# Optimization experiments

Hardware: AMD Instinct MI355X
Metric: run time of the kernel (lower is better)

Reference implementation:

```python
import jax, jax.numpy as jnp
import numpy as np

NLAT, NLON = 64, 64
CIN = 512
HEADS = 8


def _cc_weights(n):
    # Clenshaw-Curtis quadrature weights on [-1, 1] for nodes cos(k*pi/(n-1)),
    # as used by torch-harmonics for the 'equiangular' grid. Weights sum to 2.
    N = n - 1
    theta = np.pi * np.arange(n) / N
    m = N // 2
    j = np.arange(1, m + 1)
    b = np.where(2 * j == N, 1.0, 2.0)
    S = (b / (4.0 * j ** 2 - 1.0))[None, :] * np.cos(2.0 * j[None, :] * theta[:, None])
    w = 1.0 - S.sum(axis=1)
    c = np.full(n, 2.0)
    c[0] = 1.0
    c[-1] = 1.0
    return c * w / N


def _log_quad_weights(nlat, nlon):
    # _precompute_latitudes flips nodes/weights; then 2*pi*w/nlon tiled over lon.
    w = _cc_weights(nlat)[::-1].copy()
    qw = 2.0 * np.pi * w / nlon                       # (nlat,)
    qw = np.tile(qw[:, None], (1, nlon)).reshape(-1)  # (nlat*nlon,)
    return jnp.asarray(np.log(qw), dtype=jnp.float32)


def setup_inputs() -> dict:
    key = jax.random.key(0)
    ks = jax.random.split(key, 5)
    s_qkv = float(np.sqrt(3.0 / CIN))   # scale for q/k/v 1x1-conv weights
    s_proj = float(np.sqrt(3.0 / CIN))  # out_channels == CIN
    u = lambda k, sh, s: jax.random.uniform(k, sh, jnp.float32, -s, s)
    return dict(
        query=jax.random.normal(ks[0], (1, CIN, NLAT, NLON), jnp.float32),
        q_w=u(ks[1], (CIN, CIN), s_qkv), q_b=jnp.zeros((CIN,), jnp.float32),
        k_w=u(ks[2], (CIN, CIN), s_qkv), k_b=jnp.zeros((CIN,), jnp.float32),
        v_w=u(ks[3], (CIN, CIN), s_qkv), v_b=jnp.zeros((CIN,), jnp.float32),
        p_w=u(ks[4], (CIN, CIN), s_proj), p_b=jnp.zeros((CIN,), jnp.float32),
        log_quad_weights=_log_quad_weights(NLAT, NLON),
    )


def reference(query, q_w, q_b, k_w, k_b, v_w, v_b, p_w, p_b, log_quad_weights):
    B, C, H, W = query.shape
    hd = C // HEADS  # head dim (k_channels == out_channels == in_channels)

    def proj_tokens(x, w, b):
        # 1x1 conv == channel matmul, then split heads and flatten H*W tokens
        y = jnp.einsum('bihw,oi->bohw', x, w) + b[None, :, None, None]
        return y.reshape(B, HEADS, -1, H, W).transpose(0, 1, 3, 4, 2).reshape(B, HEADS, H * W, -1)

    q = proj_tokens(query, q_w, q_b)  # (B, heads, HW, hd)
    k = proj_tokens(query, k_w, k_b)  # self-attention: key/value default to query
    v = proj_tokens(query, v_w, v_b)

    scale = 1.0 / jnp.sqrt(jnp.asarray(hd, dtype=q.dtype))
    # additive log-quadrature bias over keys (broadcast over batch/head/query)
    logits = jnp.einsum('bhqd,bhkd->bhqk', q, k) * scale + log_quad_weights[None, None, None, :]
    attn = jax.nn.softmax(logits, axis=-1)
    out = jnp.einsum('bhqk,bhkd->bhqd', attn, v)          # (B, heads, HW, hd)
    out = out.transpose(0, 1, 3, 2).reshape(B, HEADS * hd, H, W)
    return jnp.einsum('bihw,oi->bohw', out, p_w) + p_b[None, :, None, None]
```

## Files before the change

### kernel.cpp

```cpp
#include <hip/hip_runtime.h>

typedef unsigned short u16;
typedef unsigned int u32;
typedef __bf16 bf16x8 __attribute__((ext_vector_type(8)));
typedef float f32x4 __attribute__((ext_vector_type(4)));
typedef unsigned short u16x4 __attribute__((ext_vector_type(4)));

#define LOG2E 1.4426950408889634f

#if __has_builtin(__builtin_amdgcn_exp2f)
#define EXP2F(x) __builtin_amdgcn_exp2f(x)
#else
#define EXP2F(x) exp2f(x)
#endif

__device__ __forceinline__ u16 f2bf(float f) {
    union { float f; u32 u; } a; a.f = f;
    u32 u = a.u;
    u += 0x7FFFu + ((u >> 16) & 1u);
    return (u16)(u >> 16);
}
__device__ __forceinline__ bf16x8 ldg8(const u16* p) {
    return *reinterpret_cast<const bf16x8*>(p);
}
#if __has_builtin(__builtin_amdgcn_cvt_pk_bf16_f32)
__device__ __forceinline__ u32 pack2(float a, float b) {
    auto r = __builtin_amdgcn_cvt_pk_bf16_f32(a, b);
    return __builtin_bit_cast(u32, r);
}
#else
__device__ __forceinline__ u32 pack2(float a, float b) {
    u32 ua = __float_as_uint(a) + 0x8000u;
    u32 ub = __float_as_uint(b) + 0x8000u;
    return __builtin_amdgcn_perm(ub, ua, 0x07060302);
}
#endif
__device__ __forceinline__ void async16(const void* g, void* l) {
    __builtin_amdgcn_global_load_lds(
        (const __attribute__((address_space(1))) u32*)g,
        (__attribute__((address_space(3))) u32*)l, 16, 0, 0);
}

#define MFMA16(a, b, c) __builtin_amdgcn_mfma_f32_16x16x32_bf16((a), (b), (c), 0, 0, 0)

__global__ __launch_bounds__(256) void prep(const float* __restrict__ X,
                                            u16* __restrict__ Xt,
                                            const float* __restrict__ s0,
                                            const float* __restrict__ s1,
                                            const float* __restrict__ s2,
                                            const float* __restrict__ s3,
                                            u16* __restrict__ Wqkv,
                                            u16* __restrict__ Wp,
                                            const float* __restrict__ lqw,
                                            float* __restrict__ lqw2g) {
    __shared__ u16 tile[64][65];
    const int tid = threadIdx.x;
    const int y = blockIdx.y;

    if (y < 8) {
        const int t0 = blockIdx.x * 64;
        const int c0 = y * 64;
#pragma unroll
        for (int i = 0; i < 16; ++i) {
            int idx = tid + i * 256;
            int r = idx >> 6, cc = idx & 63;
            tile[r][cc] = f2bf(X[(size_t)(c0 + r) * 4096 + t0 + cc]);
        }
        __syncthreads();
#pragma unroll
        for (int i = 0; i < 16; ++i) {
            int idx = tid + i * 256;
            int tr = idx >> 6, cc = idx & 63;
            Xt[(size_t)(t0 + tr) * 512 + c0 + cc] = tile[cc][tr];
        }
    } else if (y < 12) {
        const int m = y - 8;
        const float* s = (m == 0) ? s0 : (m == 1) ? s1 : (m == 2) ? s2 : s3;
        u16* d = (m == 3) ? Wp : Wqkv + (size_t)m * 262144;
#pragma unroll
        for (int j = 0; j < 4; ++j) {
            int i = blockIdx.x * 1024 + j * 256 + tid;
            float4 v = reinterpret_cast<const float4*>(s)[i];
            u16x4 o;
            o[0] = f2bf(v.x); o[1] = f2bf(v.y); o[2] = f2bf(v.z); o[3] = f2bf(v.w);
            reinterpret_cast<u16x4*>(d)[i] = o;
        }
    } else {
        if (blockIdx.x < 4) {
            int i = blockIdx.x * 256 + tid;
            float4 v = reinterpret_cast<const float4*>(lqw)[i];
            v.x *= LOG2E; v.y *= LOG2E; v.z *= LOG2E; v.w *= LOG2E;
            reinterpret_cast<float4*>(lqw2g)[i] = v;
        }
    }
}

__global__ __launch_bounds__(512, 2) void qkv_gemm(const u16* __restrict__ Wqkv,
                                                   const u16* __restrict__ Xt,
                                                   const float* __restrict__ qb,
                                                   const float* __restrict__ kb,
                                                   const float* __restrict__ vb,
                                                   u16* __restrict__ Qt,
                                                   u16* __restrict__ Kt,
                                                   u16* __restrict__ Vp) {
    __shared__ __align__(16) u16 Al[2][128 * 32];
    __shared__ __align__(16) u16 Bl[2][128 * 32];

    const int tid = threadIdx.x;
    const int w = tid >> 6, lane = tid & 63;
    const int quad = lane >> 4, lm = lane & 15;
    const int wm = w & 1, wn = w >> 1;
    const int n0 = blockIdx.x * 128;
    const int my = blockIdx.y;
    const int m0 = my * 128;

    const int arow = lane >> 2;
    const int sch = (lane & 3) ^ ((lane >> 3) & 3);
    const u16* agp = Wqkv + (size_t)(m0 + w * 16 + arow) * 512 + sch * 8;
    const u16* bgp = Xt + (size_t)(n0 + w * 16 + arow) * 512 + sch * 8;

    async16(agp, &Al[0][w * 16 * 32]);
    async16(bgp, &Bl[0][w * 16 * 32]);
    agp += 32; bgp += 32;

    const int FOFF = lm * 64 + ((quad ^ ((lm >> 1) & 3)) << 4);

    f32x4 acc[4][2];
#pragma unroll
    for (int mt = 0; mt < 4; ++mt)
#pragma unroll
        for (int bt = 0; bt < 2; ++bt) acc[mt][bt] = (f32x4){0.f, 0.f, 0.f, 0.f};

    __syncthreads();

    for (int s = 0; s < 16; ++s) {
        const int buf = s & 1;
        if (s < 15) {
            async16(agp, &Al[buf ^ 1][w * 16 * 32]);
            async16(bgp, &Bl[buf ^ 1][w * 16 * 32]);
            agp += 32; bgp += 32;
        }
        const char* Ab = (const char*)&Al[buf][0];
        const char* Bb = (const char*)&Bl[buf][0];
        bf16x8 af[4], bfr[2];
#pragma unroll
        for (int mt = 0; mt < 4; ++mt)
            af[mt] = *(const bf16x8*)(Ab + wm * 4096 + mt * 1024 + FOFF);
#pragma unroll
        for (int bt = 0; bt < 2; ++bt)
            bfr[bt] = *(const bf16x8*)(Bb + wn * 2048 + bt * 1024 + FOFF);
#pragma unroll
        for (int mt = 0; mt < 4; ++mt)
#pragma unroll
            for (int bt = 0; bt < 2; ++bt)
                acc[mt][bt] = MFMA16(af[mt], bfr[bt], acc[mt][bt]);
        __syncthreads();
    }

    const int mat = my >> 2;
    const float* bias = (mat == 0) ? qb : (mat == 1) ? kb : vb;
    const int chbase = (my & 3) * 128 + wm * 64 + quad * 4;

    if (mat < 2) {
        u16* out = mat ? Kt : Qt;
        const float sc = mat ? 1.0f : 0.125f * LOG2E;
#pragma unroll
        for (int mt = 0; mt < 4; ++mt) {
            const int ch = chbase + mt * 16;
            float4 bv = *(const float4*)(bias + ch);
            float bvf[4] = {bv.x, bv.y, bv.z, bv.w};
#pragma unroll
            for (int bt = 0; bt < 2; ++bt) {
                int tok = n0 + wn * 32 + bt * 16 + lm;
                u16x4 pk;
#pragma unroll
                for (int r = 0; r < 4; ++r)
                    pk[r] = f2bf((acc[mt][bt][r] + bvf[r]) * sc);
                *(u16x4*)(out + (size_t)tok * 512 + ch) = pk;
            }
        }
    } else {
#pragma unroll
        for (int mt = 0; mt < 4; ++mt) {
            const int ch = chbase + mt * 16;
            float4 bv = *(const float4*)(bias + ch);
            float bvf[4] = {bv.x, bv.y, bv.z, bv.w};
#pragma unroll
            for (int bt = 0; bt < 2; ++bt) {
                int g = bt * 16 + lm;
                int col = n0 + wn * 32 + 8 * ((g >> 2) & 3) + 4 * ((g >> 4) & 1) + (g & 3);
#pragma unroll
                for (int r = 0; r < 4; ++r)
                    Vp[(size_t)(ch + r) * 4096 + col] = f2bf(acc[mt][bt][r] + bvf[r]);
            }
        }
    }
}

__global__ __launch_bounds__(256, 2) void out_gemm(const u16* __restrict__ Wp,
                                                   const u16* __restrict__ Ot,
                                                   const float* __restrict__ pb,
                                                   float* __restrict__ out) {
    __shared__ __align__(16) u16 Al[2][128 * 32];
    __shared__ __align__(16) u16 Bl[2][64 * 32];

    const int tid = threadIdx.x;
    const int w = tid >> 6, lane = tid & 63;
    const int quad = lane >> 4, lm = lane & 15;
    const int wm = w & 1, wn = w >> 1;
    const int n0 = blockIdx.x * 64;
    const int m0 = blockIdx.y * 128;

    const int arow = lane >> 2;
    const int sch = (lane & 3) ^ ((lane >> 3) & 3);
    const u16* agp0 = Wp + (size_t)(m0 + w * 16 + arow) * 512 + sch * 8;
    const u16* agp1 = agp0 + (size_t)64 * 512;
    const u16* bgp = Ot + (size_t)(n0 + w * 16 + arow) * 512 + sch * 8;

    async16(agp0, &Al[0][w * 16 * 32]);
    async16(agp1, &Al[0][(64 + w * 16) * 32]);
    async16(bgp, &Bl[0][w * 16 * 32]);
    agp0 += 32; agp1 += 32; bgp += 32;

    const int FOFF = lm * 64 + ((quad ^ ((lm >> 1) & 3)) << 4);

    f32x4 acc[4][2];
#pragma unroll
    for (int mt = 0; mt < 4; ++mt)
#pragma unroll
        for (int bt = 0; bt < 2; ++bt) acc[mt][bt] = (f32x4){0.f, 0.f, 0.f, 0.f};

    __syncthreads();

    for (int s = 0; s < 16; ++s) {
        const int buf = s & 1;
        if (s < 15) {
            async16(agp0, &Al[buf ^ 1][w * 16 * 32]);
            async16(agp1, &Al[buf ^ 1][(64 + w * 16) * 32]);
            async16(bgp, &Bl[buf ^ 1][w * 16 * 32]);
            agp0 += 32; agp1 += 32; bgp += 32;
        }
        const char* Ab = (const char*)&Al[buf][0];
        const char* Bb = (const char*)&Bl[buf][0];
        bf16x8 af[4], bfr[2];
#pragma unroll
        for (int mt = 0; mt < 4; ++mt)
            af[mt] = *(const bf16x8*)(Ab + wm * 4096 + mt * 1024 + FOFF);
#pragma unroll
        for (int bt = 0; bt < 2; ++bt)
            bfr[bt] = *(const bf16x8*)(Bb + wn * 2048 + bt * 1024 + FOFF);
#pragma unroll
        for (int mt = 0; mt < 4; ++mt)
#pragma unroll
            for (int bt = 0; bt < 2; ++bt)
                acc[mt][bt] = MFMA16(af[mt], bfr[bt], acc[mt][bt]);
        __syncthreads();
    }

#pragma unroll
    for (int mt = 0; mt < 4; ++mt) {
        const int ch = m0 + wm * 64 + mt * 16 + quad * 4;
        float4 bv = *(const float4*)(pb + ch);
        float bvf[4] = {bv.x, bv.y, bv.z, bv.w};
#pragma unroll
        for (int bt = 0; bt < 2; ++bt) {
            int tok = n0 + wn * 32 + bt * 16 + lm;
#pragma unroll
            for (int r = 0; r < 4; ++r)
                out[(size_t)(ch + r) * 4096 + tok] = acc[mt][bt][r] + bvf[r];
        }
    }
}

#define WAITVM(N) asm volatile("s_waitcnt vmcnt(" #N ")" ::: "memory")

__global__ __launch_bounds__(256, 2) void flash_attn(const u16* __restrict__ Qt,
                                                     const u16* __restrict__ Kt,
                                                     const u16* __restrict__ Vp,
                                                     const float* __restrict__ lqw2g,
                                                     u16* __restrict__ Ot) {
    __shared__ __align__(16) char smem[65536];

    const int tid = threadIdx.x;
    const int w = tid >> 6, lane = tid & 63;
    const int quad = lane >> 4, lm = lane & 15;
    const int bid = blockIdx.x;
    const int h = bid & 7, hq = h * 64;
    const int q0 = (bid >> 3) * 64;
    const int kstart = w * 1024;

    char* kvw = smem + w * 16384;

    const int srow = lane >> 3;
    const int schunk = (lane & 7) ^ srow;
    const u16* kg = Kt + (size_t)(kstart + srow) * 512 + hq + schunk * 8;
    const u16* vg = Vp + (size_t)(hq + 2 * srow + (schunk >> 2)) * 4096 +
                    kstart + (schunk & 3) * 8;

    bf16x8 bq0[4], bq1[4];
#pragma unroll
    for (int s = 0; s < 4; ++s) {
        const u16* qb = Qt + (size_t)(q0 + s * 16 + lm) * 512 + hq + quad * 8;
        bq0[s] = ldg8(qb);
        bq1[s] = ldg8(qb + 32);
    }

    f32x4 breg0 = *(const f32x4*)(lqw2g + kstart + quad * 4);
    f32x4 breg1 = *(const f32x4*)(lqw2g + kstart + 16 + quad * 4);
    const float* bptr = lqw2g + kstart + 32 + quad * 4;

    const int A0 = lm * 128 + ((quad ^ (lm & 7)) << 4);
    const int A1 = A0 ^ 64;
    const int AV = (lm >> 1) * 128 +
                   (((4 * (lm & 1) + quad) ^ ((lm >> 1) & 7)) << 4);

#define STAGEBLK(DST)                                                          \
    {                                                                          \
        char* nb = (DST);                                                      \
        async16(kg, nb);                                                       \
        async16(kg + 8 * 512, nb + 1024);                                      \
        async16(kg + 16 * 512, nb + 2048);                                     \
        async16(kg + 24 * 512, nb + 3072);                                     \
        async16(vg, nb + 4096);                                                \
        async16(vg + (size_t)16 * 4096, nb + 5120);                            \
        async16(vg + (size_t)32 * 4096, nb + 6144);                            \
        async16(vg + (size_t)48 * 4096, nb + 7168);                            \
        kg += 32 * 512; vg += 32;                                              \
    }

    STAGEBLK(kvw)
    STAGEBLK(kvw + 8192)

    union { u32 u[4]; bf16x8 v; } onesu;
    onesu.u[0] = onesu.u[1] = onesu.u[2] = onesu.u[3] = 0x3F803F80u;
    const bf16x8 onesv = onesu.v;

    f32x4 acc_o[4][4];
#pragma unroll
    for (int mt = 0; mt < 4; ++mt)
#pragma unroll
        for (int s = 0; s < 4; ++s) acc_o[mt][s] = (f32x4){0.f, 0.f, 0.f, 0.f};
    f32x4 acc_l[4];
#pragma unroll
    for (int s = 0; s < 4; ++s) acc_l[s] = (f32x4){0.f, 0.f, 0.f, 0.f};

    int bufsel = 0;

#define BODY(WN, DOBIAS, DOSTAGE)                                              \
    {                                                                          \
        WAITVM(WN);                                                            \
        const char* Kb = kvw + bufsel;                                         \
        const char* Vb = Kb + 4096;                                            \
        bf16x8 k00 = *(const bf16x8*)(Kb + A0);                                \
        bf16x8 k01 = *(const bf16x8*)(Kb + A1);                                \
        bf16x8 k10 = *(const bf16x8*)(Kb + 2048 + A0);                         \
        bf16x8 k11 = *(const bf16x8*)(Kb + 2048 + A1);                         \
        bf16x8 vf0 = *(const bf16x8*)(Vb + AV);                                \
        bf16x8 vf1 = *(const bf16x8*)(Vb + 1024 + AV);                         \
        bf16x8 vf2 = *(const bf16x8*)(Vb + 2048 + AV);                         \
        bf16x8 vf3 = *(const bf16x8*)(Vb + 3072 + AV);                         \
        u32 bbu[4][4];                                                         \
        _Pragma("unroll")                                                      \
        for (int s = 0; s < 4; ++s) {                                          \
            f32x4 a = MFMA16(k00, bq0[s], breg0);                              \
            a = MFMA16(k01, bq1[s], a);                                        \
            bbu[s][0] = pack2(EXP2F(a[0]), EXP2F(a[1]));                       \
            bbu[s][1] = pack2(EXP2F(a[2]), EXP2F(a[3]));                       \
        }                                                                      \
        _Pragma("unroll")                                                      \
        for (int s = 0; s < 4; ++s) {                                          \
            f32x4 a = MFMA16(k10, bq0[s], breg1);                              \
            a = MFMA16(k11, bq1[s], a);                                        \
            bbu[s][2] = pack2(EXP2F(a[0]), EXP2F(a[1]));                       \
            bbu[s][3] = pack2(EXP2F(a[2]), EXP2F(a[3]));                       \
        }                                                                      \
        if (DOBIAS) {                                                          \
            breg0 = *(const f32x4*)(bptr);                                     \
            breg1 = *(const f32x4*)(bptr + 16);                                \
            bptr += 32;                                                        \
        }                                                                      \
        union { u32 u[4]; bf16x8 v; } bb[4];                                   \
        _Pragma("unroll")                                                      \
        for (int s = 0; s < 4; ++s) {                                          \
            bb[s].u[0] = bbu[s][0]; bb[s].u[1] = bbu[s][1];                    \
            bb[s].u[2] = bbu[s][2]; bb[s].u[3] = bbu[s][3];                    \
        }                                                                      \
        _Pragma("unroll")                                                      \
        for (int s = 0; s < 4; ++s) {                                          \
            acc_o[0][s] = MFMA16(vf0, bb[s].v, acc_o[0][s]);                   \
            acc_o[1][s] = MFMA16(vf1, bb[s].v, acc_o[1][s]);                   \
            acc_o[2][s] = MFMA16(vf2, bb[s].v, acc_o[2][s]);                   \
            acc_o[3][s] = MFMA16(vf3, bb[s].v, acc_o[3][s]);                   \
            acc_l[s] = MFMA16(onesv, bb[s].v, acc_l[s]);                       \
        }                                                                      \
        if (DOSTAGE) STAGEBLK(kvw + bufsel)                                    \
        bufsel ^= 8192;                                                        \
    }

    BODY(8, true, true)
    for (int t = 1; t < 30; ++t)
        BODY(10, true, true)
    BODY(10, true, false)
    BODY(2, false, false)

#undef BODY
#undef STAGEBLK

    __syncthreads();
    float* mbuf = (float*)smem;
    if (w != 0) {
        float* ob = mbuf + (w - 1) * 4096;
#pragma unroll
        for (int s = 0; s < 4; ++s) {
            const int r = s * 16 + lm;
#pragma unroll
            for (int mt = 0; mt < 4; ++mt) {
                const int sl = (mt * 4 + quad) ^ lm;
                *(f32x4*)(ob + r * 64 + sl * 4) = acc_o[mt][s];
            }
        }
        if (quad == 0) {
#pragma unroll
            for (int s = 0; s < 4; ++s)
                mbuf[12288 + (w - 1) * 64 + s * 16 + lm] = acc_l[s][0];
        }
    }
    __syncthreads();
    if (w != 0) return;

#pragma unroll
    for (int s = 0; s < 4; ++s) {
        const int r = s * 16 + lm;
        float lsum = acc_l[s][0];
#pragma unroll
        for (int p = 0; p < 3; ++p)
            lsum += mbuf[12288 + p * 64 + r];
        const float inv = 1.0f / lsum;
#pragma unroll
        for (int mt = 0; mt < 4; ++mt) {
            const int sl = (mt * 4 + quad) ^ lm;
            f32x4 o = acc_o[mt][s];
#pragma unroll
            for (int p = 0; p < 3; ++p)
                o += *(const f32x4*)(mbuf + p * 4096 + r * 64 + sl * 4);
            u16x4 pkv;
#pragma unroll
            for (int r2 = 0; r2 < 4; ++r2)
                pkv[r2] = f2bf(o[r2] * inv);
            *reinterpret_cast<u16x4*>(Ot + (size_t)(q0 + r) * 512 +
                                      hq + mt * 16 + quad * 4) = pkv;
        }
    }
}

extern "C" void kernel_launch(void* const* d_in, const int* in_sizes, int n_in,
                              void* d_out, int out_size, void* d_ws, size_t ws_size,
                              hipStream_t stream) {
    (void)in_sizes; (void)n_in; (void)out_size; (void)ws_size;
    const float* X   = (const float*)d_in[0];
    const float* qw  = (const float*)d_in[1];
    const float* qb  = (const float*)d_in[2];
    const float* kw  = (const float*)d_in[3];
    const float* kb  = (const float*)d_in[4];
    const float* vw  = (const float*)d_in[5];
    const float* vb  = (const float*)d_in[6];
    const float* pw  = (const float*)d_in[7];
    const float* pb  = (const float*)d_in[8];
    const float* lqw = (const float*)d_in[9];

    const size_t E = (size_t)4096 * 512;
    const size_t WE = (size_t)512 * 512;
    u16* Xt    = (u16*)d_ws;
    u16* Qt    = Xt + E;
    u16* Kt    = Qt + E;
    u16* Vp    = Kt + E;
    u16* Wqkv  = Vp + E;
    u16* Wp    = Wqkv + 3 * WE;
    float* lqw2g = (float*)(Wp + WE);
    u16* Ot    = Xt;

    prep<<<dim3(64, 13), dim3(256), 0, stream>>>(X, Xt, qw, kw, vw, pw,
                                                 Wqkv, Wp, lqw, lqw2g);
    qkv_gemm<<<dim3(32, 12), dim3(512), 0, stream>>>(Wqkv, Xt, qb, kb, vb, Qt, Kt, Vp);
    flash_attn<<<dim3(512), dim3(256), 0, stream>>>(Qt, Kt, Vp, lqw2g, Ot);
    out_gemm<<<dim3(64, 4), dim3(256), 0, stream>>>(Wp, Ot, pb, (float*)d_out);
}
```

Measured before the change: 78.59 us.

## Split flash attention keys across 8 waves and load V directly from global

The attention block grows from 4 to 8 waves, each handling 512 keys instead of 1024, and the launch bounds rise to 512 threads with 4 blocks per CU. V fragments are now read straight from global memory into registers rather than staged through LDS, so only K is double-buffered in shared memory. The K prefetch is issued earlier in each iteration. The cross-wave reduction runs in two passes to fit the smaller shared buffer. This is meant to raise parallelism and occupancy and cut LDS traffic, at the cost of uncached-looking global V loads on the critical path, register pressure under the tighter launch bound, and extra synchronisation in the reduction.

```diff
diff --git a/kernel.cpp b/kernel.cpp
--- a/kernel.cpp
+++ b/kernel.cpp
@@ -274,7 +274,7 @@
 
 #define WAITVM(N) asm volatile("s_waitcnt vmcnt(" #N ")" ::: "memory")
 
-__global__ __launch_bounds__(256, 2) void flash_attn(const u16* __restrict__ Qt,
+__global__ __launch_bounds__(512, 4) void flash_attn(const u16* __restrict__ Qt,
                                                      const u16* __restrict__ Kt,
                                                      const u16* __restrict__ Vp,
                                                      const float* __restrict__ lqw2g,
@@ -287,15 +287,15 @@
     const int bid = blockIdx.x;
     const int h = bid & 7, hq = h * 64;
     const int q0 = (bid >> 3) * 64;
-    const int kstart = w * 1024;
-
-    char* kvw = smem + w * 16384;
+    const int kstart = w * 512;
+
+    char* kvw = smem + w * 8192;
 
     const int srow = lane >> 3;
     const int schunk = (lane & 7) ^ srow;
     const u16* kg = Kt + (size_t)(kstart + srow) * 512 + hq + schunk * 8;
-    const u16* vg = Vp + (size_t)(hq + 2 * srow + (schunk >> 2)) * 4096 +
-                    kstart + (schunk & 3) * 8;
+
+    const u16* vp = Vp + (size_t)(hq + lm) * 4096 + kstart + quad * 8;
 
     bf16x8 bq0[4], bq1[4];
 #pragma unroll
@@ -311,25 +311,19 @@
 
     const int A0 = lm * 128 + ((quad ^ (lm & 7)) << 4);
     const int A1 = A0 ^ 64;
-    const int AV = (lm >> 1) * 128 +
-                   (((4 * (lm & 1) + quad) ^ ((lm >> 1) & 7)) << 4);
-
-#define STAGEBLK(DST)                                                          \
+
+#define STAGEK(DST)                                                            \
     {                                                                          \
         char* nb = (DST);                                                      \
         async16(kg, nb);                                                       \
         async16(kg + 8 * 512, nb + 1024);                                      \
         async16(kg + 16 * 512, nb + 2048);                                     \
         async16(kg + 24 * 512, nb + 3072);                                     \
-        async16(vg, nb + 4096);                                                \
-        async16(vg + (size_t)16 * 4096, nb + 5120);                            \
-        async16(vg + (size_t)32 * 4096, nb + 6144);                            \
-        async16(vg + (size_t)48 * 4096, nb + 7168);                            \
-        kg += 32 * 512; vg += 32;                                              \
-    }
-
-    STAGEBLK(kvw)
-    STAGEBLK(kvw + 8192)
+        kg += 32 * 512;                                                        \
+    }
+
+    STAGEK(kvw)
+    STAGEK(kvw + 4096)
 
     union { u32 u[4]; bf16x8 v; } onesu;
     onesu.u[0] = onesu.u[1] = onesu.u[2] = onesu.u[3] = 0x3F803F80u;
@@ -350,15 +344,15 @@
     {                                                                          \
         WAITVM(WN);                                                            \
         const char* Kb = kvw + bufsel;                                         \
-        const char* Vb = Kb + 4096;                                            \
+        bf16x8 vf0 = ldg8(vp);                                                 \
+        bf16x8 vf1 = ldg8(vp + (size_t)16 * 4096);                             \
+        bf16x8 vf2 = ldg8(vp + (size_t)32 * 4096);                             \
+        bf16x8 vf3 = ldg8(vp + (size_t)48 * 4096);                             \
+        vp += 32;                                                              \
         bf16x8 k00 = *(const bf16x8*)(Kb + A0);                                \
         bf16x8 k01 = *(const bf16x8*)(Kb + A1);                                \
         bf16x8 k10 = *(const bf16x8*)(Kb + 2048 + A0);                         \
         bf16x8 k11 = *(const bf16x8*)(Kb + 2048 + A1);                         \
-        bf16x8 vf0 = *(const bf16x8*)(Vb + AV);                                \
-        bf16x8 vf1 = *(const bf16x8*)(Vb + 1024 + AV);                         \
-        bf16x8 vf2 = *(const bf16x8*)(Vb + 2048 + AV);                         \
-        bf16x8 vf3 = *(const bf16x8*)(Vb + 3072 + AV);                         \
         u32 bbu[4][4];                                                         \
         _Pragma("unroll")                                                      \
         for (int s = 0; s < 4; ++s) {                                          \
@@ -379,6 +373,7 @@
             breg1 = *(const f32x4*)(bptr + 16);                                \
             bptr += 32;                                                        \
         }                                                                      \
+        if (DOSTAGE) STAGEK(kvw + bufsel)                                      \
         union { u32 u[4]; bf16x8 v; } bb[4];                                   \
         _Pragma("unroll")                                                      \
         for (int s = 0; s < 4; ++s) {                                          \
@@ -393,36 +388,64 @@
             acc_o[3][s] = MFMA16(vf3, bb[s].v, acc_o[3][s]);                   \
             acc_l[s] = MFMA16(onesv, bb[s].v, acc_l[s]);                       \
         }                                                                      \
-        if (DOSTAGE) STAGEBLK(kvw + bufsel)                                    \
-        bufsel ^= 8192;                                                        \
-    }
-
-    BODY(8, true, true)
-    for (int t = 1; t < 30; ++t)
-        BODY(10, true, true)
-    BODY(10, true, false)
-    BODY(2, false, false)
+        bufsel ^= 4096;                                                        \
+    }
+
+    BODY(4, true, true)
+    for (int t = 1; t < 15; ++t)
+        BODY(10, true, (t <= 13))
+    BODY(6, false, false)
 
 #undef BODY
-#undef STAGEBLK
+#undef STAGEK
 
     __syncthreads();
     float* mbuf = (float*)smem;
+    float* lbuf = mbuf + 7 * 2048;
+
     if (w != 0) {
-        float* ob = mbuf + (w - 1) * 4096;
+        float* ob = mbuf + (w - 1) * 2048;
 #pragma unroll
         for (int s = 0; s < 4; ++s) {
             const int r = s * 16 + lm;
 #pragma unroll
-            for (int mt = 0; mt < 4; ++mt) {
-                const int sl = (mt * 4 + quad) ^ lm;
-                *(f32x4*)(ob + r * 64 + sl * 4) = acc_o[mt][s];
+            for (int mt = 0; mt < 2; ++mt) {
+                const int sl = (mt * 4 + quad) ^ (lm & 7);
+                *(f32x4*)(ob + r * 32 + sl * 4) = acc_o[mt][s];
             }
         }
-        if (quad == 0) {
+        if (quad == 0)
 #pragma unroll
             for (int s = 0; s < 4; ++s)
-                mbuf[12288 + (w - 1) * 64 + s * 16 + lm] = acc_l[s][0];
+                lbuf[(w - 1) * 64 + s * 16 + lm] = acc_l[s][0];
+    }
+    __syncthreads();
+    if (w == 0) {
+#pragma unroll
+        for (int s = 0; s < 4; ++s) {
+            const int r = s * 16 + lm;
+#pragma unroll
+            for (int p = 0; p < 7; ++p) {
+#pragma unroll
+                for (int mt = 0; mt < 2; ++mt) {
+                    const int sl = (mt * 4 + quad) ^ (lm & 7);
+                    acc_o[mt][s] += *(const f32x4*)(mbuf + p * 2048 + r * 32 + sl * 4);
+                }
+                acc_l[s][0] += lbuf[p * 64 + r];
+            }
+        }
+    }
+    __syncthreads();
+    if (w != 0) {
+        float* ob = mbuf + (w - 1) * 2048;
+#pragma unroll
+        for (int s = 0; s < 4; ++s) {
+            const int r = s * 16 + lm;
+#pragma unroll
+            for (int mt = 2; mt < 4; ++mt) {
+                const int sl = ((mt - 2) * 4 + quad) ^ (lm & 7);
+                *(f32x4*)(ob + r * 32 + sl * 4) = acc_o[mt][s];
+            }
         }
     }
     __syncthreads();
@@ -431,22 +454,20 @@
 #pragma unroll
     for (int s = 0; s < 4; ++s) {
         const int r = s * 16 + lm;
-        float lsum = acc_l[s][0];
-#pragma unroll
-        for (int p = 0; p < 3; ++p)
-            lsum += mbuf[12288 + p * 64 + r];
-        const float inv = 1.0f / lsum;
+#pragma unroll
+        for (int p = 0; p < 7; ++p)
+#pragma unroll
+            for (int mt = 2; mt < 4; ++mt) {
+                const int sl = ((mt - 2) * 4 + quad) ^ (lm & 7);
+                acc_o[mt][s] += *(const f32x4*)(mbuf + p * 2048 + r * 32 + sl * 4);
+            }
+        const float inv = 1.0f / acc_l[s][0];
 #pragma unroll
         for (int mt = 0; mt < 4; ++mt) {
-            const int sl = (mt * 4 + quad) ^ lm;
-            f32x4 o = acc_o[mt][s];
-#pragma unroll
-            for (int p = 0; p < 3; ++p)
-                o += *(const f32x4*)(mbuf + p * 4096 + r * 64 + sl * 4);
             u16x4 pkv;
 #pragma unroll
             for (int r2 = 0; r2 < 4; ++r2)
-                pkv[r2] = f2bf(o[r2] * inv);
+                pkv[r2] = f2bf(acc_o[mt][s][r2] * inv);
             *reinterpret_cast<u16x4*>(Ot + (size_t)(q0 + r) * 512 +
                                       hq + mt * 16 + quad * 4) = pkv;
         }
@@ -482,6 +503,6 @@
     prep<<<dim3(64, 13), dim3(256), 0, stream>>>(X, Xt, qw, kw, vw, pw,
                                                  Wqkv, Wp, lqw, lqw2g);
     qkv_gemm<<<dim3(32, 12), dim3(512), 0, stream>>>(Wqkv, Xt, qb, kb, vb, Qt, Kt, Vp);
-    flash_attn<<<dim3(512), dim3(256), 0, stream>>>(Qt, Kt, Vp, lqw2g, Ot);
+    flash_attn<<<dim3(512), dim3(512), 0, stream>>>(Qt, Kt, Vp, lqw2g, Ot);
     out_gemm<<<dim3(64, 4), dim3(256), 0, stream>>>(Wp, Ot, pb, (float*)d_out);
 }
```

Result: slower. 210.2 us (+167.4%).

## Share K/V tiles across two query-halves with 8-wave blocks and barrier-synced staging

Applied to the files above, without the earlier changes.

The flash attention kernel now uses 512-thread blocks covering 128 queries. Pairs of waves share each K/V shared-memory buffer: one wave stages K, the other stages V, and s_barrier calls synchronise the double-buffered pipeline. This halves global K/V traffic per query. The row-sum MFMA against a ones vector is replaced by scalar accumulation of the exponentials. The final cross-wave reduction is split into two passes so it fits in shared memory, which adds barriers and halves the grid to 256 blocks.

```diff
diff --git a/kernel.cpp b/kernel.cpp
--- a/kernel.cpp
+++ b/kernel.cpp
@@ -273,8 +273,10 @@
 }
 
 #define WAITVM(N) asm volatile("s_waitcnt vmcnt(" #N ")" ::: "memory")
-
-__global__ __launch_bounds__(256, 2) void flash_attn(const u16* __restrict__ Qt,
+#define SBAR() __builtin_amdgcn_s_barrier()
+#define SCHEDB() __builtin_amdgcn_sched_barrier(0)
+
+__global__ __launch_bounds__(512, 2) void flash_attn(const u16* __restrict__ Qt,
                                                      const u16* __restrict__ Kt,
                                                      const u16* __restrict__ Vp,
                                                      const float* __restrict__ lqw2g,
@@ -284,12 +286,13 @@
     const int tid = threadIdx.x;
     const int w = tid >> 6, lane = tid & 63;
     const int quad = lane >> 4, lm = lane & 15;
+    const int qh = w & 1, kq = w >> 1;
     const int bid = blockIdx.x;
     const int h = bid & 7, hq = h * 64;
-    const int q0 = (bid >> 3) * 64;
-    const int kstart = w * 1024;
-
-    char* kvw = smem + w * 16384;
+    const int q0 = (bid >> 3) * 128;
+    const int kstart = kq * 1024;
+
+    char* kvb = smem + kq * 16384;
 
     const int srow = lane >> 3;
     const int schunk = (lane & 7) ^ srow;
@@ -300,7 +303,7 @@
     bf16x8 bq0[4], bq1[4];
 #pragma unroll
     for (int s = 0; s < 4; ++s) {
-        const u16* qb = Qt + (size_t)(q0 + s * 16 + lm) * 512 + hq + quad * 8;
+        const u16* qb = Qt + (size_t)(q0 + qh * 64 + s * 16 + lm) * 512 + hq + quad * 8;
         bq0[s] = ldg8(qb);
         bq1[s] = ldg8(qb + 32);
     }
@@ -314,42 +317,48 @@
     const int AV = (lm >> 1) * 128 +
                    (((4 * (lm & 1) + quad) ^ ((lm >> 1) & 7)) << 4);
 
-#define STAGEBLK(DST)                                                          \
+#define STAGE(DST)                                                             \
     {                                                                          \
         char* nb = (DST);                                                      \
-        async16(kg, nb);                                                       \
-        async16(kg + 8 * 512, nb + 1024);                                      \
-        async16(kg + 16 * 512, nb + 2048);                                     \
-        async16(kg + 24 * 512, nb + 3072);                                     \
-        async16(vg, nb + 4096);                                                \
-        async16(vg + (size_t)16 * 4096, nb + 5120);                            \
-        async16(vg + (size_t)32 * 4096, nb + 6144);                            \
-        async16(vg + (size_t)48 * 4096, nb + 7168);                            \
-        kg += 32 * 512; vg += 32;                                              \
-    }
-
-    STAGEBLK(kvw)
-    STAGEBLK(kvw + 8192)
-
-    union { u32 u[4]; bf16x8 v; } onesu;
-    onesu.u[0] = onesu.u[1] = onesu.u[2] = onesu.u[3] = 0x3F803F80u;
-    const bf16x8 onesv = onesu.v;
+        if (qh == 0) {                                                         \
+            async16(kg, nb);                                                   \
+            async16(kg + 8 * 512, nb + 1024);                                  \
+            async16(kg + 16 * 512, nb + 2048);                                 \
+            async16(kg + 24 * 512, nb + 3072);                                 \
+            kg += 32 * 512;                                                    \
+        } else {                                                               \
+            async16(vg, nb + 4096);                                            \
+            async16(vg + (size_t)16 * 4096, nb + 5120);                        \
+            async16(vg + (size_t)32 * 4096, nb + 6144);                        \
+            async16(vg + (size_t)48 * 4096, nb + 7168);                        \
+            vg += 32;                                                          \
+        }                                                                      \
+    }
+
+    STAGE(kvb)
 
     f32x4 acc_o[4][4];
 #pragma unroll
     for (int mt = 0; mt < 4; ++mt)
 #pragma unroll
         for (int s = 0; s < 4; ++s) acc_o[mt][s] = (f32x4){0.f, 0.f, 0.f, 0.f};
-    f32x4 acc_l[4];
-#pragma unroll
-    for (int s = 0; s < 4; ++s) acc_l[s] = (f32x4){0.f, 0.f, 0.f, 0.f};
+    float psum[4] = {0.f, 0.f, 0.f, 0.f};
 
     int bufsel = 0;
 
-#define BODY(WN, DOBIAS, DOSTAGE)                                              \
+#define BODY(WN, DO)                                                           \
     {                                                                          \
+        f32x4 bnext0, bnext1;                                                  \
+        if (DO) {                                                              \
+            STAGE(kvb + (bufsel ^ 8192))                                       \
+            bnext0 = *(const f32x4*)(bptr);                                    \
+            bnext1 = *(const f32x4*)(bptr + 16);                               \
+            bptr += 32;                                                        \
+        }                                                                      \
         WAITVM(WN);                                                            \
-        const char* Kb = kvw + bufsel;                                         \
+        SBAR();                                                                \
+        SCHEDB();                                                              \
+        const char* Kb = kvb + bufsel;                                         \
         const char* Vb = Kb + 4096;                                            \
         bf16x8 k00 = *(const bf16x8*)(Kb + A0);                                \
         bf16x8 k01 = *(const bf16x8*)(Kb + A1);                                \
@@ -359,31 +368,23 @@
         bf16x8 vf1 = *(const bf16x8*)(Vb + 1024 + AV);                         \
         bf16x8 vf2 = *(const bf16x8*)(Vb + 2048 + AV);                         \
         bf16x8 vf3 = *(const bf16x8*)(Vb + 3072 + AV);                         \
-        u32 bbu[4][4];                                                         \
+        union { u32 u[4]; bf16x8 v; } bb[4];                                   \
         _Pragma("unroll")                                                      \
         for (int s = 0; s < 4; ++s) {                                          \
             f32x4 a = MFMA16(k00, bq0[s], breg0);                              \
             a = MFMA16(k01, bq1[s], a);                                        \
-            bbu[s][0] = pack2(EXP2F(a[0]), EXP2F(a[1]));                       \
-            bbu[s][1] = pack2(EXP2F(a[2]), EXP2F(a[3]));                       \
-        }                                                                      \
-        _Pragma("unroll")                                                      \
-        for (int s = 0; s < 4; ++s) {                                          \
-            f32x4 a = MFMA16(k10, bq0[s], breg1);                              \
-            a = MFMA16(k11, bq1[s], a);                                        \
-            bbu[s][2] = pack2(EXP2F(a[0]), EXP2F(a[1]));                       \
-            bbu[s][3] = pack2(EXP2F(a[2]), EXP2F(a[3]));                       \
-        }                                                                      \
-        if (DOBIAS) {                                                          \
-            breg0 = *(const f32x4*)(bptr);                                     \
-            breg1 = *(const f32x4*)(bptr + 16);                                \
-            bptr += 32;                                                        \
-        }                                                                      \
-        union { u32 u[4]; bf16x8 v; } bb[4];                                   \
-        _Pragma("unroll")                                                      \
-        for (int s = 0; s < 4; ++s) {                                          \
-            bb[s].u[0] = bbu[s][0]; bb[s].u[1] = bbu[s][1];                    \
-            bb[s].u[2] = bbu[s][2]; bb[s].u[3] = bbu[s][3];                    \
+            float e0 = EXP2F(a[0]), e1 = EXP2F(a[1]);                          \
+            float e2 = EXP2F(a[2]), e3 = EXP2F(a[3]);                          \
+            psum[s] += (e0 + e1) + (e2 + e3);                                  \
+            bb[s].u[0] = pack2(e0, e1);                                        \
+            bb[s].u[1] = pack2(e2, e3);                                        \
+            f32x4 c = MFMA16(k10, bq0[s], breg1);                              \
+            c = MFMA16(k11, bq1[s], c);                                        \
+            float f0 = EXP2F(c[0]), f1 = EXP2F(c[1]);                          \
+            float f2 = EXP2F(c[2]), f3 = EXP2F(c[3]);                          \
+            psum[s] += (f0 + f1) + (f2 + f3);                                  \
+            bb[s].u[2] = pack2(f0, f1);                                        \
+            bb[s].u[3] = pack2(f2, f3);                                        \
         }                                                                      \
         _Pragma("unroll")                                                      \
         for (int s = 0; s < 4; ++s) {                                          \
@@ -391,63 +392,97 @@
             acc_o[1][s] = MFMA16(vf1, bb[s].v, acc_o[1][s]);                   \
             acc_o[2][s] = MFMA16(vf2, bb[s].v, acc_o[2][s]);                   \
             acc_o[3][s] = MFMA16(vf3, bb[s].v, acc_o[3][s]);                   \
-            acc_l[s] = MFMA16(onesv, bb[s].v, acc_l[s]);                       \
         }                                                                      \
-        if (DOSTAGE) STAGEBLK(kvw + bufsel)                                    \
+        SBAR();                                                                \
+        SCHEDB();                                                              \
+        if (DO) { breg0 = bnext0; breg1 = bnext1; }                            \
         bufsel ^= 8192;                                                        \
     }
 
-    BODY(8, true, true)
-    for (int t = 1; t < 30; ++t)
-        BODY(10, true, true)
-    BODY(10, true, false)
-    BODY(2, false, false)
+    for (int t = 0; t < 31; ++t)
+        BODY(6, true)
+    BODY(2, false)
 
 #undef BODY
-#undef STAGEBLK
-
+#undef STAGE
+
+    float* mbuf = (float*)smem;
+    float* lbuf = mbuf + 3 * 4096;
+
+#pragma unroll
+    for (int s = 0; s < 4; ++s)
+        lbuf[(qh * 64 + s * 16 + lm) * 20 + kq * 4 + quad] = psum[s];
+
+    if (kq != 0) {
+        float* ob = mbuf + (kq - 1) * 4096;
+#pragma unroll
+        for (int s = 0; s < 4; ++s) {
+            const int row = qh * 64 + s * 16 + lm;
+#pragma unroll
+            for (int mt = 0; mt < 2; ++mt) {
+                const int sl = (mt * 4 + quad) ^ (lm & 7);
+                *(f32x4*)(ob + row * 32 + sl * 4) = acc_o[mt][s];
+            }
+        }
+    }
     __syncthreads();
-    float* mbuf = (float*)smem;
-    if (w != 0) {
-        float* ob = mbuf + (w - 1) * 4096;
+    float invs[4];
+    if (kq == 0) {
 #pragma unroll
         for (int s = 0; s < 4; ++s) {
-            const int r = s * 16 + lm;
-#pragma unroll
-            for (int mt = 0; mt < 4; ++mt) {
-                const int sl = (mt * 4 + quad) ^ lm;
-                *(f32x4*)(ob + r * 64 + sl * 4) = acc_o[mt][s];
+            const int row = qh * 64 + s * 16 + lm;
+            f32x4 lv = (f32x4){0.f, 0.f, 0.f, 0.f};
+#pragma unroll
+            for (int j = 0; j < 4; ++j)
+                lv += *(const f32x4*)(lbuf + row * 20 + j * 4);
+            invs[s] = 1.0f / ((lv[0] + lv[1]) + (lv[2] + lv[3]));
+#pragma unroll
+            for (int mt = 0; mt < 2; ++mt) {
+                const int sl = (mt * 4 + quad) ^ (lm & 7);
+                f32x4 o = acc_o[mt][s];
+#pragma unroll
+                for (int p = 0; p < 3; ++p)
+                    o += *(const f32x4*)(mbuf + p * 4096 + row * 32 + sl * 4);
+                u16x4 pkv;
+#pragma unroll
+                for (int r = 0; r < 4; ++r)
+                    pkv[r] = f2bf(o[r] * invs[s]);
+                *reinterpret_cast<u16x4*>(Ot + (size_t)(q0 + row) * 512 +
+                                          hq + mt * 16 + quad * 4) = pkv;
             }
         }
-        if (quad == 0) {
-#pragma unroll
-            for (int s = 0; s < 4; ++s)
-                mbuf[12288 + (w - 1) * 64 + s * 16 + lm] = acc_l[s][0];
-        }
     }
     __syncthreads();
-    if (w != 0) return;
+    if (kq != 0) {
+        float* ob = mbuf + (kq - 1) * 4096;
+#pragma unroll
+        for (int s = 0; s < 4; ++s) {
+            const int row = qh * 64 + s * 16 + lm;
+#pragma unroll
+            for (int mt = 2; mt < 4; ++mt) {
+                const int sl = ((mt - 2) * 4 + quad) ^ (lm & 7);
+                *(f32x4*)(ob + row * 32 + sl * 4) = acc_o[mt][s];
+            }
+        }
+    }
+    __syncthreads();
+    if (kq != 0) return;
 
 #pragma unroll
     for (int s = 0; s < 4; ++s) {
-        const int r = s * 16 + lm;
-        float lsum = acc_l[s][0];
-#pragma unroll
-        for (int p = 0; p < 3; ++p)
-            lsum += mbuf[12288 + p * 64 + r];
-        const float inv = 1.0f / lsum;
-#pragma unroll
-        for (int mt = 0; mt < 4; ++mt) {
-            const int sl = (mt * 4 + quad) ^ lm;
+        const int row = qh * 64 + s * 16 + lm;
+#pragma unroll
+        for (int mt = 2; mt < 4; ++mt) {
+            const int sl = ((mt - 2) * 4 + quad) ^ (lm & 7);
             f32x4 o = acc_o[mt][s];
 #pragma unroll
             for (int p = 0; p < 3; ++p)
-                o += *(const f32x4*)(mbuf + p * 4096 + r * 64 + sl * 4);
+                o += *(const f32x4*)(mbuf + p * 4096 + row * 32 + sl * 4);
             u16x4 pkv;
 #pragma unroll
-            for (int r2 = 0; r2 < 4; ++r2)
-                pkv[r2] = f2bf(o[r2] * inv);
-            *reinterpret_cast<u16x4*>(Ot + (size_t)(q0 + r) * 512 +
+            for (int r = 0; r < 4; ++r)
+                pkv[r] = f2bf(o[r] * invs[s]);
+            *reinterpret_cast<u16x4*>(Ot + (size_t)(q0 + row) * 512 +
                                       hq + mt * 16 + quad * 4) = pkv;
         }
     }
@@ -482,6 +517,6 @@
     prep<<<dim3(64, 13), dim3(256), 0, stream>>>(X, Xt, qw, kw, vw, pw,
                                                  Wqkv, Wp, lqw, lqw2g);
     qkv_gemm<<<dim3(32, 12), dim3(512), 0, stream>>>(Wqkv, Xt, qb, kb, vb, Qt, Kt, Vp);
-    flash_attn<<<dim3(512), dim3(256), 0, stream>>>(Qt, Kt, Vp, lqw2g, Ot);
+    flash_attn<<<dim3(256), dim3(512), 0, stream>>>(Qt, Kt, Vp, lqw2g, Ot);
     out_gemm<<<dim3(64, 4), dim3(256), 0, stream>>>(Wp, Ot, pb, (float*)d_out);
 }
```

New measurement: 86.83 us. 10.5% more time.

## Software-pipeline PV MFMAs one key block behind QK and exp

Applied to the files above, without the earlier changes.

Restructures the attention inner loop so the P·V and row-sum MFMAs for the previous key block are issued before the QK MFMAs and exp of the current block. The V fragments and packed probabilities are carried across iterations, and a drain step after the loop handles the last block. This lets matrix-core work overlap the transcendental and pack work instead of stalling on the exp results. In exchange it keeps extra registers live across iterations (4 V fragments plus 4 packed P vectors), which may raise register pressure or lower occupancy.

```diff
diff --git a/kernel.cpp b/kernel.cpp
--- a/kernel.cpp
+++ b/kernel.cpp
@@ -344,9 +344,11 @@
 #pragma unroll
     for (int s = 0; s < 4; ++s) acc_l[s] = (f32x4){0.f, 0.f, 0.f, 0.f};
 
+    union { u32 u[4]; bf16x8 v; } pb_[4];
+    bf16x8 pv0, pv1, pv2, pv3;
     int bufsel = 0;
 
-#define BODY(WN, DOBIAS, DOSTAGE)                                              \
+#define BODY(WN, DOBIAS, DOSTAGE, DOPV)                                        \
     {                                                                          \
         WAITVM(WN);                                                            \
         const char* Kb = kvw + bufsel;                                         \
@@ -355,56 +357,61 @@
         bf16x8 k01 = *(const bf16x8*)(Kb + A1);                                \
         bf16x8 k10 = *(const bf16x8*)(Kb + 2048 + A0);                         \
         bf16x8 k11 = *(const bf16x8*)(Kb + 2048 + A1);                         \
-        bf16x8 vf0 = *(const bf16x8*)(Vb + AV);                                \
-        bf16x8 vf1 = *(const bf16x8*)(Vb + 1024 + AV);                         \
-        bf16x8 vf2 = *(const bf16x8*)(Vb + 2048 + AV);                         \
-        bf16x8 vf3 = *(const bf16x8*)(Vb + 3072 + AV);                         \
-        u32 bbu[4][4];                                                         \
+        bf16x8 nv0 = *(const bf16x8*)(Vb + AV);                                \
+        bf16x8 nv1 = *(const bf16x8*)(Vb + 1024 + AV);                         \
+        bf16x8 nv2 = *(const bf16x8*)(Vb + 2048 + AV);                         \
+        bf16x8 nv3 = *(const bf16x8*)(Vb + 3072 + AV);                         \
+        if (DOPV) {                                                            \
+            _Pragma("unroll")                                                  \
+            for (int s = 0; s < 4; ++s) {                                      \
+                acc_o[0][s] = MFMA16(pv0, pb_[s].v, acc_o[0][s]);              \
+                acc_o[1][s] = MFMA16(pv1, pb_[s].v, acc_o[1][s]);              \
+                acc_o[2][s] = MFMA16(pv2, pb_[s].v, acc_o[2][s]);              \
+                acc_o[3][s] = MFMA16(pv3, pb_[s].v, acc_o[3][s]);              \
+                acc_l[s] = MFMA16(onesv, pb_[s].v, acc_l[s]);                  \
+            }                                                                  \
+        }                                                                      \
         _Pragma("unroll")                                                      \
         for (int s = 0; s < 4; ++s) {                                          \
             f32x4 a = MFMA16(k00, bq0[s], breg0);                              \
             a = MFMA16(k01, bq1[s], a);                                        \
-            bbu[s][0] = pack2(EXP2F(a[0]), EXP2F(a[1]));                       \
-            bbu[s][1] = pack2(EXP2F(a[2]), EXP2F(a[3]));                       \
+            pb_[s].u[0] = pack2(EXP2F(a[0]), EXP2F(a[1]));                     \
+            pb_[s].u[1] = pack2(EXP2F(a[2]), EXP2F(a[3]));                     \
         }                                                                      \
         _Pragma("unroll")                                                      \
         for (int s = 0; s < 4; ++s) {                                          \
-            f32x4 a = MFMA16(k10, bq0[s], breg1);                              \
-            a = MFMA16(k11, bq1[s], a);                                        \
-            bbu[s][2] = pack2(EXP2F(a[0]), EXP2F(a[1]));                       \
-            bbu[s][3] = pack2(EXP2F(a[2]), EXP2F(a[3]));                       \
+            f32x4 c = MFMA16(k10, bq0[s], breg1);                              \
+            c = MFMA16(k11, bq1[s], c);                                        \
+            pb_[s].u[2] = pack2(EXP2F(c[0]), EXP2F(c[1]));                     \
+            pb_[s].u[3] = pack2(EXP2F(c[2]), EXP2F(c[3]));                     \
         }                                                                      \
         if (DOBIAS) {                                                          \
             breg0 = *(const f32x4*)(bptr);                                     \
             breg1 = *(const f32x4*)(bptr + 16);                                \
             bptr += 32;                                                        \
         }                                                                      \
-        union { u32 u[4]; bf16x8 v; } bb[4];                                   \
-        _Pragma("unroll")                                                      \
-        for (int s = 0; s < 4; ++s) {                                          \
-            bb[s].u[0] = bbu[s][0]; bb[s].u[1] = bbu[s][1];                    \
-            bb[s].u[2] = bbu[s][2]; bb[s].u[3] = bbu[s][3];                    \
-        }                                                                      \
-        _Pragma("unroll")                                                      \
-        for (int s = 0; s < 4; ++s) {                                          \
-            acc_o[0][s] = MFMA16(vf0, bb[s].v, acc_o[0][s]);                   \
-            acc_o[1][s] = MFMA16(vf1, bb[s].v, acc_o[1][s]);                   \
-            acc_o[2][s] = MFMA16(vf2, bb[s].v, acc_o[2][s]);                   \
-            acc_o[3][s] = MFMA16(vf3, bb[s].v, acc_o[3][s]);                   \
-            acc_l[s] = MFMA16(onesv, bb[s].v, acc_l[s]);                       \
-        }                                                                      \
+        pv0 = nv0; pv1 = nv1; pv2 = nv2; pv3 = nv3;                            \
         if (DOSTAGE) STAGEBLK(kvw + bufsel)                                    \
         bufsel ^= 8192;                                                        \
     }
 
-    BODY(8, true, true)
+    BODY(8, true, true, false)
     for (int t = 1; t < 30; ++t)
-        BODY(10, true, true)
-    BODY(10, true, false)
-    BODY(2, false, false)
+        BODY(10, true, true, true)
+    BODY(10, true, false, true)
+    BODY(2, false, false, true)
 
 #undef BODY
 #undef STAGEBLK
+
+#pragma unroll
+    for (int s = 0; s < 4; ++s) {
+        acc_o[0][s] = MFMA16(pv0, pb_[s].v, acc_o[0][s]);
+        acc_o[1][s] = MFMA16(pv1, pb_[s].v, acc_o[1][s]);
+        acc_o[2][s] = MFMA16(pv2, pb_[s].v, acc_o[2][s]);
+        acc_o[3][s] = MFMA16(pv3, pb_[s].v, acc_o[3][s]);
+        acc_l[s] = MFMA16(onesv, pb_[s].v, acc_l[s]);
+    }
 
     __syncthreads();
     float* mbuf = (float*)smem;
```

Measured after the change: 77.75 us. No clear change (-1.1%).
